# Optimization experiments

Hardware: AMD Instinct MI355X
Metric: run time of the kernel (lower is better)

## Reference

```python
import jax, jax.numpy as jnp
import numpy as np

N_LAYERS = 4


def setup_inputs() -> dict:
    key = jax.random.key(0)
    k1, k2 = jax.random.split(key)
    data = jax.random.normal(k1, (100000, 512), dtype=jnp.float32)
    codebooks = jax.random.normal(k2, (N_LAYERS, 1024, 512), dtype=jnp.float32) * 0.1
    return {"data": data, "codebooks": codebooks}


def _nearest(residual, cb):
    # squared euclidean distances [N, K]; argmin identical to cdist argmin
    x2 = jnp.sum(residual * residual, axis=1, keepdims=True)        # [N,1]
    c2 = jnp.sum(cb * cb, axis=1)[None, :]                          # [1,K]
    d2 = x2 + c2 - 2.0 * (residual @ cb.T)                          # [N,K]
    return jnp.argmin(d2, axis=1)


def reference(data, codebooks):
    """encode (iterative residual quantization) then decode. Returns (codes, reconstructed)."""
    residual = data
    codes = []
    recon = jnp.zeros_like(data)
    for l in range(N_LAYERS):  # small fixed layer count, sequential dependency
        cb = codebooks[l]                       # [K,F]
        idx = _nearest(residual, cb)            # [N]
        q = cb[idx]                             # gather [N,F]
        residual = residual - q
        recon = recon + q
        codes.append(idx)
    codes = jnp.stack(codes, axis=1).astype(jnp.int64)  # [N, n_layers]
    return codes, recon
```

## Files before the change

kernel.cpp:

```cpp
#include <hip/hip_runtime.h>
#include <hip/hip_bf16.h>
#include <math.h>

#define NL 4
#define KC 1024
#define FD 512
#define MT 16
#define BLK 256
#define RS 516
#define NCAND 6

typedef __attribute__((ext_vector_type(8))) short short8;
typedef __attribute__((ext_vector_type(4))) float f32x4;

__device__ __forceinline__ short bf16c(float x) {
  __hip_bfloat16 h = __float2bfloat16(x);
  return *reinterpret_cast<short*>(&h);
}

__device__ __forceinline__ float np_chunk_partial(const float* p, int l16) {
  float pm[8];
#pragma unroll
  for (int m = 0; m < 8; m++) {
    float v = p[m * 16 + l16];
    pm[m] = __fmul_rn(v, v);
  }
  float a = __fadd_rn(__fadd_rn(pm[0], pm[1]), __fadd_rn(pm[2], pm[3]));
  float b = __fadd_rn(__fadd_rn(pm[4], pm[5]), __fadd_rn(pm[6], pm[7]));
  return __fadd_rn(a, b);
}

__global__ __launch_bounds__(BLK) void c2_kernel(const float* __restrict__ cb,
                                                 float* __restrict__ c2) {
  int wid  = (blockIdx.x * BLK + threadIdx.x) >> 6;
  int lane = threadIdx.x & 63;
  if (wid >= NL * KC) return;
  const float* row = cb + (size_t)wid * FD;
  int chunk = lane >> 4, l16 = lane & 15;
  float part = np_chunk_partial(row + chunk * 128, l16);
  part = __fadd_rn(part, __shfl_xor(part, 8));
  part = __fadd_rn(part, __shfl_xor(part, 4));
  part = __fadd_rn(part, __shfl_xor(part, 2));
  part = __fadd_rn(part, __shfl_xor(part, 1));
  float s1 = __fadd_rn(part, __shfl_xor(part, 16));
  float s  = __fadd_rn(s1, __shfl_xor(s1, 32));
  if (lane == 0) c2[wid] = s;
}

__global__ __launch_bounds__(BLK) void swz_kernel(const float* __restrict__ cb,
                                                  short* __restrict__ cbw) {
  int g = blockIdx.x * BLK + threadIdx.x;
  int w = g >> 6, lane = g & 63;
  if (w >= NL * 16 * 64) return;
  int l = w >> 10, c = (w >> 6) & 15, T = w & 63;
  int kidx = T * 16 + (lane & 15);
  int f0   = c * 32 + ((lane >> 4) << 3);
  const float* src = cb + (((size_t)l * KC + kidx) * FD + f0);
  short8 v;
#pragma unroll
  for (int j = 0; j < 8; j++) v[j] = bf16c(src[j]);
  *(short8*)(cbw + (size_t)w * 512 + lane * 8) = v;
}

__global__ __launch_bounds__(BLK, 2) void rq_kernel(
    const float* __restrict__ data, const float* __restrict__ cb,
    const float* __restrict__ c2g, const short* __restrict__ cbw,
    float* __restrict__ codes_out, float* __restrict__ recon_out, int N) {
  __shared__ float resid[MT * RS];
  __shared__ float pool_d[MT * 128];
  __shared__ int   pool_k[MT * 128];
  __shared__ float mrg_d[MT * 24];
  __shared__ int   mrg_k[MT * 24];
  __shared__ float sh_part[MT * 64];
  __shared__ float sh_x2[MT];
  __shared__ float sc_d[MT * NCAND];
  __shared__ int   sc_k[MT * NCAND];
  __shared__ int   cand_k[MT * NCAND];
  __shared__ int   hist_k[NL * MT];

  const int t    = threadIdx.x;
  const int n0   = blockIdx.x * MT;
  if (n0 >= N) return;
  const int wv   = t >> 6;
  const int lane = t & 63;
  const int l15  = lane & 15;
  const int lq   = lane >> 4;

#pragma unroll
  for (int q = 0; q < 8; q++) {
    int id = t + BLK * q;
    int m = id >> 7, c4 = id & 127;
    int mg = n0 + m; if (mg > N - 1) mg = N - 1;
    *(float4*)&resid[m * RS + c4 * 4] =
        *(const float4*)&data[(size_t)mg * FD + c4 * 4];
  }
  __syncthreads();

  for (int l = 0; l < NL; l++) {
    const float* cbl = cb + (size_t)l * KC * FD;

    {
      int row = t >> 4, j16 = t & 15;
#pragma unroll
      for (int c = 0; c < 4; c++)
        sh_part[(row * 4 + c) * 16 + j16] =
            np_chunk_partial(&resid[row * RS + c * 128], j16);
    }
    __syncthreads();
    if (t < MT) {
      const float* P = &sh_part[t * 64];
      float b[4];
#pragma unroll
      for (int c = 0; c < 4; c++) {
        float u[8];
#pragma unroll
        for (int j2 = 0; j2 < 8; j2++)
          u[j2] = __fadd_rn(P[c * 16 + j2], P[c * 16 + j2 + 8]);
        float v[4];
#pragma unroll
        for (int j2 = 0; j2 < 4; j2++) v[j2] = __fadd_rn(u[j2], u[j2 + 4]);
        b[c] = __fadd_rn(__fadd_rn(v[0], v[2]), __fadd_rn(v[1], v[3]));
      }
      sh_x2[t] = __fadd_rn(__fadd_rn(b[0], b[1]), __fadd_rn(b[2], b[3]));
    }
    __syncthreads();

    f32x4 acc[16];
#pragma unroll
    for (int tt = 0; tt < 16; tt++) acc[tt] = (f32x4)0.f;

    float c2f[16];
#pragma unroll
    for (int tt = 0; tt < 16; tt++)
      c2f[tt] = c2g[l * KC + wv * 256 + tt * 16 + l15];

    for (int ch = 0; ch < 16; ch++) {
      float4 alo = *(const float4*)&resid[l15 * RS + ch * 32 + lq * 8];
      float4 ahi = *(const float4*)&resid[l15 * RS + ch * 32 + lq * 8 + 4];
      short8 av;
      av[0] = bf16c(alo.x); av[1] = bf16c(alo.y);
      av[2] = bf16c(alo.z); av[3] = bf16c(alo.w);
      av[4] = bf16c(ahi.x); av[5] = bf16c(ahi.y);
      av[6] = bf16c(ahi.z); av[7] = bf16c(ahi.w);
      const short8* bp =
          (const short8*)(cbw + (((size_t)l * 16 + ch) * 64 + wv * 16) * 512);
#pragma unroll
      for (int tt = 0; tt < 16; tt++) {
        short8 bv = bp[tt * 64 + lane];
        acc[tt] = __builtin_amdgcn_mfma_f32_16x16x32_bf16(av, bv, acc[tt],
                                                          0, 0, 0);
      }
    }

#pragma unroll
    for (int g = 0; g < 4; g++) {
      float b1 = INFINITY, b2 = INFINITY; int k1 = 0x7fffffff, k2 = 0x7fffffff;
#pragma unroll
      for (int tt = 0; tt < 16; tt++) {
        float s = c2f[tt] - 2.0f * acc[tt][g];
        int k = wv * 256 + tt * 16 + l15;
        if (s < b1) { b2 = b1; k2 = k1; b1 = s; k1 = k; }
        else if (s < b2) { b2 = s; k2 = k; }
      }
      int r = lq * 4 + g;
      int base = r * 128 + wv * 32 + l15 * 2;
      pool_d[base] = b1; pool_k[base] = k1;
      pool_d[base + 1] = b2; pool_k[base + 1] = k2;
    }
    __syncthreads();

    if (t < 64) {
      int r = t >> 2, seg = t & 3;
      float cd[NCAND]; int ck[NCAND];
#pragma unroll
      for (int j = 0; j < NCAND; j++) { cd[j] = INFINITY; ck[j] = 0x7fffffff; }
      for (int e = 0; e < 32; e++) {
        int idx = seg * 32 + ((e + t) & 31);
        float d = pool_d[r * 128 + idx];
        int   k = pool_k[r * 128 + idx];
#pragma unroll
        for (int j = 0; j < NCAND; j++) {
          bool better = (d < cd[j]) || (d == cd[j] && k < ck[j]);
          if (better) { float td = cd[j]; cd[j] = d; d = td;
                        int   tk = ck[j]; ck[j] = k; k = tk; }
        }
      }
#pragma unroll
      for (int j = 0; j < NCAND; j++) {
        mrg_d[r * 24 + seg * NCAND + j] = cd[j];
        mrg_k[r * 24 + seg * NCAND + j] = ck[j];
      }
    }
    __syncthreads();

    if (t < MT) {
      float cd[NCAND]; int ck[NCAND];
#pragma unroll
      for (int j = 0; j < NCAND; j++) { cd[j] = INFINITY; ck[j] = 0x7fffffff; }
      for (int e = 0; e < 24; e++) {
        float d = mrg_d[t * 24 + e];
        int   k = mrg_k[t * 24 + e];
#pragma unroll
        for (int j = 0; j < NCAND; j++) {
          bool better = (d < cd[j]) || (d == cd[j] && k < ck[j]);
          if (better) { float td = cd[j]; cd[j] = d; d = td;
                        int   tk = ck[j]; ck[j] = k; k = tk; }
        }
      }
#pragma unroll
      for (int j = 0; j < NCAND; j++) cand_k[t * NCAND + j] = ck[j];
    }
    __syncthreads();

    if (t < MT * NCAND) {
      int r = t / NCAND, c = t - r * NCAND;
      int k = cand_k[r * NCAND + c];
      const float* cw = cbl + (size_t)k * FD;
      float sum = 0.f;
#pragma unroll 8
      for (int i = 0; i < 128; i++) {
        float4 rv = *(const float4*)&resid[r * RS + i * 4];
        float4 qv = *(const float4*)&cw[i * 4];
        sum = __fmaf_rn(rv.x, qv.x, sum);
        sum = __fmaf_rn(rv.y, qv.y, sum);
        sum = __fmaf_rn(rv.z, qv.z, sum);
        sum = __fmaf_rn(rv.w, qv.w, sum);
      }
      float c2e = c2g[l * KC + k];
      sc_d[r * NCAND + c] = __fsub_rn(__fadd_rn(sh_x2[r], c2e),
                                      __fmul_rn(2.0f, sum));
      sc_k[r * NCAND + c] = k;
    }
    __syncthreads();

    if (t < MT) {
      float bd = INFINITY; int bk = 0x7fffffff;
#pragma unroll
      for (int c = 0; c < NCAND; c++) {
        float d = sc_d[t * NCAND + c];
        int   k = sc_k[t * NCAND + c];
        if (d < bd || (d == bd && k < bk)) { bd = d; bk = k; }
      }
      hist_k[l * MT + t] = bk;
      if (n0 + t < N) codes_out[(size_t)(n0 + t) * NL + l] = (float)bk;
    }
    __syncthreads();

    if (l < NL - 1) {
#pragma unroll
      for (int q = 0; q < 8; q++) {
        int id = t + BLK * q;
        int m = id >> 7, c4 = id & 127;
        int bk2 = hist_k[l * MT + m];
        float4 qv = *(const float4*)&cbl[(size_t)bk2 * FD + c4 * 4];
        float4 rv = *(float4*)&resid[m * RS + c4 * 4];
        rv.x = __fsub_rn(rv.x, qv.x); rv.y = __fsub_rn(rv.y, qv.y);
        rv.z = __fsub_rn(rv.z, qv.z); rv.w = __fsub_rn(rv.w, qv.w);
        *(float4*)&resid[m * RS + c4 * 4] = rv;
      }
      __syncthreads();
    }
  }

#pragma unroll
  for (int q = 0; q < 8; q++) {
    int id = t + BLK * q;
    int m = id >> 7, c4 = id & 127;
    int mg = n0 + m;
    if (mg < N) {
      float4 q0 = *(const float4*)&cb[((size_t)0 * KC + hist_k[0 * MT + m]) * FD + c4 * 4];
      float4 q1 = *(const float4*)&cb[((size_t)1 * KC + hist_k[1 * MT + m]) * FD + c4 * 4];
      float4 q2 = *(const float4*)&cb[((size_t)2 * KC + hist_k[2 * MT + m]) * FD + c4 * 4];
      float4 q3 = *(const float4*)&cb[((size_t)3 * KC + hist_k[3 * MT + m]) * FD + c4 * 4];
      float4 o;
      o.x = __fadd_rn(__fadd_rn(__fadd_rn(q0.x, q1.x), q2.x), q3.x);
      o.y = __fadd_rn(__fadd_rn(__fadd_rn(q0.y, q1.y), q2.y), q3.y);
      o.z = __fadd_rn(__fadd_rn(__fadd_rn(q0.z, q1.z), q2.z), q3.z);
      o.w = __fadd_rn(__fadd_rn(__fadd_rn(q0.w, q1.w), q2.w), q3.w);
      *(float4*)&recon_out[(size_t)mg * FD + c4 * 4] = o;
    }
  }
}

extern "C" void kernel_launch(void* const* d_in, const int* in_sizes, int n_in,
                              void* d_out, int out_size, void* d_ws, size_t ws_size,
                              hipStream_t stream) {
  const float* data = (const float*)d_in[0];
  const float* cb   = (const float*)d_in[1];
  int N = in_sizes[0] / FD;

  float* c2  = (float*)d_ws;
  short* cbw = (short*)((char*)d_ws + 16384);
  float* codes_out = (float*)d_out;
  float* recon_out = codes_out + (size_t)N * NL;

  c2_kernel<<<(NL * KC + 3) / 4, BLK, 0, stream>>>(cb, c2);
  swz_kernel<<<(NL * 16 * 64) / 4, BLK, 0, stream>>>(cb, cbw);
  int nblocks = (N + MT - 1) / MT;
  rq_kernel<<<nblocks, BLK, 0, stream>>>(data, cb, c2, cbw, codes_out,
                                         recon_out, N);
}
```

Baseline: 3.883 ms.

## Double rows per block to 32, vectorize candidate merges, accumulate recon in registers

The main kernel now handles 32 rows per 512-thread block, with two groups of four waves, each group covering 16 rows over all 1024 codes. This halves the number of blocks and the per-row overhead of the serial selection phases. The top-k merge loops now read the pool through float4/int4 loads with a padded stride. Reconstruction is accumulated in registers during each layer's residual update, which removes the final re-gather of all four codebook rows. Costs: the larger block uses more shared memory, and the register array under __launch_bounds__(512,2) may lower occupancy or cause spills.

```diff
diff --git a/kernel.cpp b/kernel.cpp
--- a/kernel.cpp
+++ b/kernel.cpp
@@ -5,9 +5,11 @@
 #define NL 4
 #define KC 1024
 #define FD 512
-#define MT 16
-#define BLK 256
+#define MT 32
+#define BLK 512
+#define HBLK 256
 #define RS 516
+#define PPS 132
 #define NCAND 6
 
 typedef __attribute__((ext_vector_type(8))) short short8;
@@ -30,9 +32,9 @@
   return __fadd_rn(a, b);
 }
 
-__global__ __launch_bounds__(BLK) void c2_kernel(const float* __restrict__ cb,
-                                                 float* __restrict__ c2) {
-  int wid  = (blockIdx.x * BLK + threadIdx.x) >> 6;
+__global__ __launch_bounds__(HBLK) void c2_kernel(const float* __restrict__ cb,
+                                                  float* __restrict__ c2) {
+  int wid  = (blockIdx.x * HBLK + threadIdx.x) >> 6;
   int lane = threadIdx.x & 63;
   if (wid >= NL * KC) return;
   const float* row = cb + (size_t)wid * FD;
@@ -47,9 +49,9 @@
   if (lane == 0) c2[wid] = s;
 }
 
-__global__ __launch_bounds__(BLK) void swz_kernel(const float* __restrict__ cb,
-                                                  short* __restrict__ cbw) {
-  int g = blockIdx.x * BLK + threadIdx.x;
+__global__ __launch_bounds__(HBLK) void swz_kernel(const float* __restrict__ cb,
+                                                   short* __restrict__ cbw) {
+  int g = blockIdx.x * HBLK + threadIdx.x;
   int w = g >> 6, lane = g & 63;
   if (w >= NL * 16 * 64) return;
   int l = w >> 10, c = (w >> 6) & 15, T = w & 63;
@@ -62,13 +64,23 @@
   *(short8*)(cbw + (size_t)w * 512 + lane * 8) = v;
 }
 
+#define INS(dval, kval) do {                                              \
+    float _d = (dval); int _k = (kval);                                   \
+    _Pragma("unroll")                                                     \
+    for (int _j = 0; _j < NCAND; _j++) {                                  \
+      bool _b = (_d < cd[_j]) || (_d == cd[_j] && _k < ck[_j]);           \
+      if (_b) { float _td = cd[_j]; cd[_j] = _d; _d = _td;                \
+                int   _tk = ck[_j]; ck[_j] = _k; _k = _tk; }              \
+    }                                                                     \
+  } while (0)
+
 __global__ __launch_bounds__(BLK, 2) void rq_kernel(
     const float* __restrict__ data, const float* __restrict__ cb,
     const float* __restrict__ c2g, const short* __restrict__ cbw,
     float* __restrict__ codes_out, float* __restrict__ recon_out, int N) {
   __shared__ float resid[MT * RS];
-  __shared__ float pool_d[MT * 128];
-  __shared__ int   pool_k[MT * 128];
+  __shared__ float pool_d[MT * PPS];
+  __shared__ int   pool_k[MT * PPS];
   __shared__ float mrg_d[MT * 24];
   __shared__ int   mrg_k[MT * 24];
   __shared__ float sh_part[MT * 64];
@@ -81,10 +93,13 @@
   const int t    = threadIdx.x;
   const int n0   = blockIdx.x * MT;
   if (n0 >= N) return;
-  const int wv   = t >> 6;
-  const int lane = t & 63;
-  const int l15  = lane & 15;
-  const int lq   = lane >> 4;
+  const int wv    = t >> 6;
+  const int lane  = t & 63;
+  const int l15   = lane & 15;
+  const int lq    = lane >> 4;
+  const int rh    = wv >> 2;
+  const int wc    = wv & 3;
+  const int rbase = rh << 4;
 
 #pragma unroll
   for (int q = 0; q < 8; q++) {
@@ -96,6 +111,8 @@
   }
   __syncthreads();
 
+  float4 rec[8];
+
   for (int l = 0; l < NL; l++) {
     const float* cbl = cb + (size_t)l * KC * FD;
 
@@ -132,18 +149,18 @@
     float c2f[16];
 #pragma unroll
     for (int tt = 0; tt < 16; tt++)
-      c2f[tt] = c2g[l * KC + wv * 256 + tt * 16 + l15];
+      c2f[tt] = c2g[l * KC + wc * 256 + tt * 16 + l15];
 
     for (int ch = 0; ch < 16; ch++) {
-      float4 alo = *(const float4*)&resid[l15 * RS + ch * 32 + lq * 8];
-      float4 ahi = *(const float4*)&resid[l15 * RS + ch * 32 + lq * 8 + 4];
+      float4 alo = *(const float4*)&resid[(rbase + l15) * RS + ch * 32 + lq * 8];
+      float4 ahi = *(const float4*)&resid[(rbase + l15) * RS + ch * 32 + lq * 8 + 4];
       short8 av;
       av[0] = bf16c(alo.x); av[1] = bf16c(alo.y);
       av[2] = bf16c(alo.z); av[3] = bf16c(alo.w);
       av[4] = bf16c(ahi.x); av[5] = bf16c(ahi.y);
       av[6] = bf16c(ahi.z); av[7] = bf16c(ahi.w);
       const short8* bp =
-          (const short8*)(cbw + (((size_t)l * 16 + ch) * 64 + wv * 16) * 512);
+          (const short8*)(cbw + (((size_t)l * 16 + ch) * 64 + wc * 16) * 512);
 #pragma unroll
       for (int tt = 0; tt < 16; tt++) {
         short8 bv = bp[tt * 64 + lane];
@@ -158,32 +175,31 @@
 #pragma unroll
       for (int tt = 0; tt < 16; tt++) {
         float s = c2f[tt] - 2.0f * acc[tt][g];
-        int k = wv * 256 + tt * 16 + l15;
+        int k = wc * 256 + tt * 16 + l15;
         if (s < b1) { b2 = b1; k2 = k1; b1 = s; k1 = k; }
         else if (s < b2) { b2 = s; k2 = k; }
       }
-      int r = lq * 4 + g;
-      int base = r * 128 + wv * 32 + l15 * 2;
+      int r = rbase + lq * 4 + g;
+      int base = r * PPS + wc * 32 + l15 * 2;
       pool_d[base] = b1; pool_k[base] = k1;
       pool_d[base + 1] = b2; pool_k[base + 1] = k2;
     }
     __syncthreads();
 
-    if (t < 64) {
+    if (t < 4 * MT) {
       int r = t >> 2, seg = t & 3;
+      const float4* pd4 = (const float4*)&pool_d[r * PPS + seg * 32];
+      const int4*   pk4 = (const int4*)  &pool_k[r * PPS + seg * 32];
+      float4 dv[8]; int4 kv[8];
+#pragma unroll
+      for (int e = 0; e < 8; e++) { dv[e] = pd4[e]; kv[e] = pk4[e]; }
       float cd[NCAND]; int ck[NCAND];
 #pragma unroll
       for (int j = 0; j < NCAND; j++) { cd[j] = INFINITY; ck[j] = 0x7fffffff; }
-      for (int e = 0; e < 32; e++) {
-        int idx = seg * 32 + ((e + t) & 31);
-        float d = pool_d[r * 128 + idx];
-        int   k = pool_k[r * 128 + idx];
-#pragma unroll
-        for (int j = 0; j < NCAND; j++) {
-          bool better = (d < cd[j]) || (d == cd[j] && k < ck[j]);
-          if (better) { float td = cd[j]; cd[j] = d; d = td;
-                        int   tk = ck[j]; ck[j] = k; k = tk; }
-        }
+#pragma unroll
+      for (int e = 0; e < 8; e++) {
+        INS(dv[e].x, kv[e].x); INS(dv[e].y, kv[e].y);
+        INS(dv[e].z, kv[e].z); INS(dv[e].w, kv[e].w);
       }
 #pragma unroll
       for (int j = 0; j < NCAND; j++) {
@@ -194,18 +210,18 @@
     __syncthreads();
 
     if (t < MT) {
+      const float4* md4 = (const float4*)&mrg_d[t * 24];
+      const int4*   mk4 = (const int4*)  &mrg_k[t * 24];
+      float4 dv[6]; int4 kv[6];
+#pragma unroll
+      for (int e = 0; e < 6; e++) { dv[e] = md4[e]; kv[e] = mk4[e]; }
       float cd[NCAND]; int ck[NCAND];
 #pragma unroll
       for (int j = 0; j < NCAND; j++) { cd[j] = INFINITY; ck[j] = 0x7fffffff; }
-      for (int e = 0; e < 24; e++) {
-        float d = mrg_d[t * 24 + e];
-        int   k = mrg_k[t * 24 + e];
-#pragma unroll
-        for (int j = 0; j < NCAND; j++) {
-          bool better = (d < cd[j]) || (d == cd[j] && k < ck[j]);
-          if (better) { float td = cd[j]; cd[j] = d; d = td;
-                        int   tk = ck[j]; ck[j] = k; k = tk; }
-        }
+#pragma unroll
+      for (int e = 0; e < 6; e++) {
+        INS(dv[e].x, kv[e].x); INS(dv[e].y, kv[e].y);
+        INS(dv[e].z, kv[e].z); INS(dv[e].w, kv[e].w);
       }
 #pragma unroll
       for (int j = 0; j < NCAND; j++) cand_k[t * NCAND + j] = ck[j];
@@ -246,20 +262,28 @@
     }
     __syncthreads();
 
-    if (l < NL - 1) {
-#pragma unroll
-      for (int q = 0; q < 8; q++) {
-        int id = t + BLK * q;
-        int m = id >> 7, c4 = id & 127;
-        int bk2 = hist_k[l * MT + m];
-        float4 qv = *(const float4*)&cbl[(size_t)bk2 * FD + c4 * 4];
+#pragma unroll
+    for (int q = 0; q < 8; q++) {
+      int id = t + BLK * q;
+      int m = id >> 7, c4 = id & 127;
+      int bk2 = hist_k[l * MT + m];
+      float4 qv = *(const float4*)&cbl[(size_t)bk2 * FD + c4 * 4];
+      if (l == 0) {
+        rec[q] = qv;
+      } else {
+        rec[q].x = __fadd_rn(rec[q].x, qv.x);
+        rec[q].y = __fadd_rn(rec[q].y, qv.y);
+        rec[q].z = __fadd_rn(rec[q].z, qv.z);
+        rec[q].w = __fadd_rn(rec[q].w, qv.w);
+      }
+      if (l < NL - 1) {
         float4 rv = *(float4*)&resid[m * RS + c4 * 4];
         rv.x = __fsub_rn(rv.x, qv.x); rv.y = __fsub_rn(rv.y, qv.y);
         rv.z = __fsub_rn(rv.z, qv.z); rv.w = __fsub_rn(rv.w, qv.w);
         *(float4*)&resid[m * RS + c4 * 4] = rv;
       }
-      __syncthreads();
-    }
+    }
+    if (l < NL - 1) __syncthreads();
   }
 
 #pragma unroll
@@ -267,18 +291,8 @@
     int id = t + BLK * q;
     int m = id >> 7, c4 = id & 127;
     int mg = n0 + m;
-    if (mg < N) {
-      float4 q0 = *(const float4*)&cb[((size_t)0 * KC + hist_k[0 * MT + m]) * FD + c4 * 4];
-      float4 q1 = *(const float4*)&cb[((size_t)1 * KC + hist_k[1 * MT + m]) * FD + c4 * 4];
-      float4 q2 = *(const float4*)&cb[((size_t)2 * KC + hist_k[2 * MT + m]) * FD + c4 * 4];
-      float4 q3 = *(const float4*)&cb[((size_t)3 * KC + hist_k[3 * MT + m]) * FD + c4 * 4];
-      float4 o;
-      o.x = __fadd_rn(__fadd_rn(__fadd_rn(q0.x, q1.x), q2.x), q3.x);
-      o.y = __fadd_rn(__fadd_rn(__fadd_rn(q0.y, q1.y), q2.y), q3.y);
-      o.z = __fadd_rn(__fadd_rn(__fadd_rn(q0.z, q1.z), q2.z), q3.z);
-      o.w = __fadd_rn(__fadd_rn(__fadd_rn(q0.w, q1.w), q2.w), q3.w);
-      *(float4*)&recon_out[(size_t)mg * FD + c4 * 4] = o;
-    }
+    if (mg < N)
+      *(float4*)&recon_out[(size_t)mg * FD + c4 * 4] = rec[q];
   }
 }
 
@@ -294,8 +308,8 @@
   float* codes_out = (float*)d_out;
   float* recon_out = codes_out + (size_t)N * NL;
 
-  c2_kernel<<<(NL * KC + 3) / 4, BLK, 0, stream>>>(cb, c2);
-  swz_kernel<<<(NL * 16 * 64) / 4, BLK, 0, stream>>>(cb, cbw);
+  c2_kernel<<<(NL * KC + 3) / 4, HBLK, 0, stream>>>(cb, c2);
+  swz_kernel<<<(NL * 16 * 64) / 4, HBLK, 0, stream>>>(cb, cbw);
   int nblocks = (N + MT - 1) / MT;
   rq_kernel<<<nblocks, BLK, 0, stream>>>(data, cb, c2, cbw, codes_out,
                                          recon_out, N);
```

Measured after the change: 3.804 ms. 2.0% less time.
